# Kernel tuning notes

Measured on AMD Instinct MI355X. Metric: run time of the kernel, lower is better.

## Reference

```python
import jax, jax.numpy as jnp
import numpy as np

N, D = 16384, 512
C = 1024

def setup_inputs() -> dict:
    key = jax.random.key(0)
    k1, k2, k3 = jax.random.split(key, 3)
    inputs = jax.random.normal(k1, (N, D), dtype=jnp.float32)
    centers = jax.random.normal(k2, (C, D), dtype=jnp.float32)
    gamma = jnp.float32(1.0 / D)  # standard RBF bandwidth
    normalization = jax.random.normal(k3, (C, C), dtype=jnp.float32) * 0.02
    return {"inputs": inputs, "centers": centers, "gamma": gamma,
            "normalization": normalization}

def gaussian_kernel(inputs, centers, gamma):
    x2 = jnp.sum(inputs * inputs, axis=-1, keepdims=True)        # [N,1]
    c2 = jnp.sum(centers * centers, axis=-1)                     # [C]
    xc = jnp.einsum('nd,cd->nc', inputs, centers)                # [N,C]
    sq_dist = jnp.maximum(x2 + c2[None, :] - 2.0 * xc, 0.0)
    return jnp.exp(-gamma * sq_dist)                             # [N,C]

def reference(inputs, centers, gamma, normalization):
    inputs = inputs.reshape(inputs.shape[0], -1)
    densities = gaussian_kernel(inputs, centers, gamma)
    return densities @ normalization                             # [N,C]
```

## Files before the change

kernel.cpp:

```cpp
#include <hip/hip_runtime.h>
#include <hip/hip_bf16.h>
#include <stdint.h>

#define N_ROWS 16384
#define D_DIM  512
#define C_DIM  1024

typedef __attribute__((ext_vector_type(4))) float f32x4;
typedef __attribute__((ext_vector_type(8))) short bf16x8;

__device__ __forceinline__ short bfbits(float x) {
  uint32_t u = __float_as_uint(x);
  uint32_t r = (u + 0x7fffu + ((u >> 16) & 1u)) >> 16;
  return (short)r;
}

__device__ __forceinline__ void gload16(const short* g, const short* l) {
  __builtin_amdgcn_global_load_lds(
      (const __attribute__((address_space(1))) void*)g,
      (__attribute__((address_space(3))) void*)l, 16, 0, 0);
}

__global__ __launch_bounds__(256) void fused_prep(
    const float* __restrict__ inputs, const float* __restrict__ centers,
    const float* __restrict__ W, short* __restrict__ inb,
    short* __restrict__ cenb, short* __restrict__ wT,
    float* __restrict__ x2, float* __restrict__ c2) {
  int bid = blockIdx.x;
  if (bid < 4096 + 256) {
    const float* src; short* dst; float* sq; int row;
    if (bid < 4096) { src = inputs; dst = inb; sq = x2; row = bid * 4 + (threadIdx.x >> 6); }
    else { src = centers; dst = cenb; sq = c2; row = (bid - 4096) * 4 + (threadIdx.x >> 6); }
    int lane = threadIdx.x & 63;
    const float4* s = reinterpret_cast<const float4*>(src + (size_t)row * D_DIM) + lane * 2;
    float4 v0 = s[0], v1 = s[1];
    float ss = v0.x*v0.x + v0.y*v0.y + v0.z*v0.z + v0.w*v0.w
             + v1.x*v1.x + v1.y*v1.y + v1.z*v1.z + v1.w*v1.w;
    bf16x8 o;
    o[0]=bfbits(v0.x); o[1]=bfbits(v0.y); o[2]=bfbits(v0.z); o[3]=bfbits(v0.w);
    o[4]=bfbits(v1.x); o[5]=bfbits(v1.y); o[6]=bfbits(v1.z); o[7]=bfbits(v1.w);
    *reinterpret_cast<bf16x8*>(dst + (size_t)row * D_DIM + lane * 8) = o;
    #pragma unroll
    for (int off = 32; off; off >>= 1) ss += __shfl_down(ss, off, 64);
    if (lane == 0) sq[row] = ss;
  } else {
    __shared__ float tile[32][33];
    int b2 = bid - 4352;
    int j0 = (b2 & 31) * 32;
    int c0 = (b2 >> 5) * 32;
    int tx = threadIdx.x & 31;
    int ty = threadIdx.x >> 5;
    #pragma unroll
    for (int i = 0; i < 32; i += 8)
      tile[ty + i][tx] = W[(size_t)(c0 + ty + i) * C_DIM + j0 + tx];
    __syncthreads();
    #pragma unroll
    for (int i = 0; i < 32; i += 8)
      wT[(size_t)(j0 + ty + i) * C_DIM + c0 + tx] = bfbits(tile[tx][ty + i]);
  }
}

template<int EPI>
__global__ __launch_bounds__(512, 2)
void gemm256(const short* __restrict__ A, const short* __restrict__ B,
             void* __restrict__ Cp, const float* __restrict__ x2,
             const float* __restrict__ c2, const float* __restrict__ gptr,
             int K) {
  __shared__ __align__(16) short lds[65536];
  short* As = lds;
  short* Bs = lds + 32768;

  const int tid  = threadIdx.x;
  const int lane = tid & 63;
  const int wid  = tid >> 6;
  const int wr = wid >> 2;
  const int wc = wid & 3;

  const int bid  = blockIdx.x;
  const int brow = (bid & 7) * 8 + (bid >> 5);
  const int bcol = (bid >> 3) & 3;
  const int row0 = brow * 256, col0 = bcol * 256;

  const int NT = K >> 6;

  const int l15 = lane & 15;
  const int lk  = (lane >> 4) * 8;
  const int sw  = (lane & 7) << 3;
  const int swHi = sw & 32, swLo = sw & 24;
  const int ca0 = swHi | (lk ^ swLo);
  const int ca1 = (swHi ^ 32) | (lk ^ swLo);
  const int aRow = (wr * 128 + l15) * 64;
  const int bRow = (wc * 64  + l15) * 64;

  const int rowL = tid >> 3;
  const int chS  = ((tid & 7) ^ (rowL & 7)) << 3;
  const short* gA = A + (size_t)(row0 + rowL) * K + chS;
  const short* gB = B + (size_t)(col0 + rowL) * K + chS;
  const int ldsT = tid * 8;

#define STG_A(buf, u, kt) gload16(gA + (size_t)((u) * 64) * K + (kt), As + (buf) * 16384 + (u) * 4096 + ldsT)
#define STG_B(buf, u, kt) gload16(gB + (size_t)((u) * 64) * K + (kt), Bs + (buf) * 16384 + (u) * 4096 + ldsT)

  f32x4 acc[8][4] = {};

  STG_A(0, 0, 0); STG_A(0, 2, 0); STG_A(0, 1, 0); STG_A(0, 3, 0);
  STG_B(0, 0, 0); STG_B(0, 1, 0); STG_B(0, 2, 0); STG_B(0, 3, 0);
  {
    const int kt1 = ((NT > 1) ? 1 : 0) << 6;
    STG_A(1, 0, kt1); STG_A(1, 2, kt1);
    STG_B(1, 0, kt1); STG_B(1, 1, kt1); STG_B(1, 2, kt1); STG_B(1, 3, kt1);
  }
  asm volatile("s_waitcnt vmcnt(6)" ::: "memory");
  __builtin_amdgcn_s_barrier();

  bf16x8 a[4], b0[4], b1[4];
  for (int t = 0; t < NT; ++t) {
    const int bsel = t & 1, nb = bsel ^ 1;
    const short* aB = As + bsel * 16384;
    const short* bB = Bs + bsel * 16384;
    const int kt1 = ((t + 1 < NT) ? (t + 1) : (NT - 1)) << 6;
    const int kt2 = ((t + 2 < NT) ? (t + 2) : (NT - 1)) << 6;

    #pragma unroll
    for (int i = 0; i < 4; ++i) a[i]  = *(const bf16x8*)(aB + aRow + i * 1024 + ca0);
    #pragma unroll
    for (int n = 0; n < 4; ++n) b0[n] = *(const bf16x8*)(bB + bRow + n * 1024 + ca0);
    STG_A(nb, 1, kt1); STG_A(nb, 3, kt1);
    __builtin_amdgcn_s_barrier();
    asm volatile("s_waitcnt lgkmcnt(0)" ::: "memory");
    __builtin_amdgcn_sched_barrier(0);
    __builtin_amdgcn_s_setprio(1);
    #pragma unroll
    for (int i = 0; i < 4; ++i)
      #pragma unroll
      for (int n = 0; n < 4; ++n)
        acc[i][n] = __builtin_amdgcn_mfma_f32_16x16x32_bf16(a[i], b0[n], acc[i][n], 0, 0, 0);
    __builtin_amdgcn_s_setprio(0);
    __builtin_amdgcn_s_barrier();

    #pragma unroll
    for (int i = 0; i < 4; ++i) a[i] = *(const bf16x8*)(aB + aRow + (4 + i) * 1024 + ca0);
    __builtin_amdgcn_s_barrier();
    asm volatile("s_waitcnt lgkmcnt(0)" ::: "memory");
    __builtin_amdgcn_sched_barrier(0);
    __builtin_amdgcn_s_setprio(1);
    #pragma unroll
    for (int i = 0; i < 4; ++i)
      #pragma unroll
      for (int n = 0; n < 4; ++n)
        acc[4 + i][n] = __builtin_amdgcn_mfma_f32_16x16x32_bf16(a[i], b0[n], acc[4 + i][n], 0, 0, 0);
    __builtin_amdgcn_s_setprio(0);
    __builtin_amdgcn_s_barrier();

    #pragma unroll
    for (int i = 0; i < 4; ++i) a[i]  = *(const bf16x8*)(aB + aRow + i * 1024 + ca1);
    #pragma unroll
    for (int n = 0; n < 4; ++n) b1[n] = *(const bf16x8*)(bB + bRow + n * 1024 + ca1);
    __builtin_amdgcn_s_barrier();
    asm volatile("s_waitcnt lgkmcnt(0)" ::: "memory");
    __builtin_amdgcn_sched_barrier(0);
    __builtin_amdgcn_s_setprio(1);
    #pragma unroll
    for (int i = 0; i < 4; ++i)
      #pragma unroll
      for (int n = 0; n < 4; ++n)
        acc[i][n] = __builtin_amdgcn_mfma_f32_16x16x32_bf16(a[i], b1[n], acc[i][n], 0, 0, 0);
    __builtin_amdgcn_s_setprio(0);
    __builtin_amdgcn_s_barrier();

    #pragma unroll
    for (int i = 0; i < 4; ++i) a[i] = *(const bf16x8*)(aB + aRow + (4 + i) * 1024 + ca1);
    STG_A(bsel, 0, kt2); STG_A(bsel, 2, kt2);
    STG_B(bsel, 0, kt2); STG_B(bsel, 1, kt2); STG_B(bsel, 2, kt2); STG_B(bsel, 3, kt2);
    asm volatile("s_waitcnt vmcnt(6)" ::: "memory");
    __builtin_amdgcn_s_barrier();
    asm volatile("s_waitcnt lgkmcnt(0)" ::: "memory");
    __builtin_amdgcn_sched_barrier(0);
    __builtin_amdgcn_s_setprio(1);
    #pragma unroll
    for (int i = 0; i < 4; ++i)
      #pragma unroll
      for (int n = 0; n < 4; ++n)
        acc[4 + i][n] = __builtin_amdgcn_mfma_f32_16x16x32_bf16(a[i], b1[n], acc[4 + i][n], 0, 0, 0);
    __builtin_amdgcn_s_setprio(0);
    __builtin_amdgcn_s_barrier();
  }

  const int colB = col0 + wc * 64 + l15;
  const int rBase = row0 + wr * 128 + ((lane >> 4) << 2);

  if constexpr (EPI == 0) {
    short* Dm = (short*)Cp;
    const float g = *gptr;
    float cc2[4];
    #pragma unroll
    for (int n = 0; n < 4; ++n) cc2[n] = c2[colB + n * 16];
    #pragma unroll
    for (int m = 0; m < 8; ++m) {
      #pragma unroll
      for (int r = 0; r < 4; ++r) {
        const int row = rBase + m * 16 + r;
        const float xr = x2[row];
        size_t base = (size_t)row * C_DIM + colB;
        #pragma unroll
        for (int n = 0; n < 4; ++n) {
          float v = fmaxf(xr + cc2[n] - 2.0f * acc[m][n][r], 0.0f);
          Dm[base + n * 16] = bfbits(__expf(-g * v));
        }
      }
    }
  } else {
    float* Dm = (float*)Cp;
    #pragma unroll
    for (int m = 0; m < 8; ++m) {
      #pragma unroll
      for (int r = 0; r < 4; ++r) {
        const int row = rBase + m * 16 + r;
        size_t base = (size_t)row * C_DIM + colB;
        #pragma unroll
        for (int n = 0; n < 4; ++n)
          Dm[base + n * 16] = acc[m][n][r];
      }
    }
  }
#undef STG_A
#undef STG_B
}

extern "C" void kernel_launch(void* const* d_in, const int* in_sizes, int n_in,
                              void* d_out, int out_size, void* d_ws, size_t ws_size,
                              hipStream_t stream) {
  const float* inputs  = (const float*)d_in[0];
  const float* centers = (const float*)d_in[1];
  const float* gamma   = (const float*)d_in[2];
  const float* norm    = (const float*)d_in[3];
  float* out = (float*)d_out;

  char* ws = (char*)d_ws;
  short* inb  = (short*)(ws);
  short* cenb = (short*)(ws + (16u << 20));
  short* wT   = (short*)(ws + (17u << 20));
  float* x2   = (float*)(ws + (19u << 20));
  float* c2   = (float*)(ws + (19u << 20) + (1u << 16));
  short* dens = (short*)(ws + (20u << 20));

  fused_prep<<<5376, 256, 0, stream>>>(inputs, centers, norm, inb, cenb, wT, x2, c2);
  gemm256<0><<<256, 512, 0, stream>>>(inb, cenb, dens, x2, c2, gamma, D_DIM);
  gemm256<1><<<256, 512, 0, stream>>>(dens, wT, out, nullptr, nullptr, nullptr, C_DIM);
}
```

Measured before the change: 154.0 us.

## Replace ping-pong barrier schedule with simple double-buffered prefetch loop

Drops the finely interleaved GEMM main loop, which had partial-tile staggered global-to-LDS loads, per-phase barriers, lgkmcnt waits and s_setprio bumps. In its place is a plain double-buffer: the whole next tile is issued up front, all four MFMA phases run back to back, then the loop waits vmcnt(0) with one barrier per iteration. This removes most barrier and sync overhead and lets the compiler schedule the LDS reads freely. The cost is losing the two-tiles-ahead prefetch depth and the explicit wave-priority interleaving, so load latency may be hidden less well.

Measured after the change: 151.4 us. About the same (-1.7%).

```diff
diff --git a/kernel.cpp b/kernel.cpp
--- a/kernel.cpp
+++ b/kernel.cpp
@@ -100,90 +100,65 @@
 
 #define STG_A(buf, u, kt) gload16(gA + (size_t)((u) * 64) * K + (kt), As + (buf) * 16384 + (u) * 4096 + ldsT)
 #define STG_B(buf, u, kt) gload16(gB + (size_t)((u) * 64) * K + (kt), Bs + (buf) * 16384 + (u) * 4096 + ldsT)
+#define STG_TILE(buf, kt) do { \
+    STG_A(buf, 0, kt); STG_A(buf, 1, kt); STG_A(buf, 2, kt); STG_A(buf, 3, kt); \
+    STG_B(buf, 0, kt); STG_B(buf, 1, kt); STG_B(buf, 2, kt); STG_B(buf, 3, kt); \
+  } while (0)
 
   f32x4 acc[8][4] = {};
 
-  STG_A(0, 0, 0); STG_A(0, 2, 0); STG_A(0, 1, 0); STG_A(0, 3, 0);
-  STG_B(0, 0, 0); STG_B(0, 1, 0); STG_B(0, 2, 0); STG_B(0, 3, 0);
-  {
-    const int kt1 = ((NT > 1) ? 1 : 0) << 6;
-    STG_A(1, 0, kt1); STG_A(1, 2, kt1);
-    STG_B(1, 0, kt1); STG_B(1, 1, kt1); STG_B(1, 2, kt1); STG_B(1, 3, kt1);
-  }
-  asm volatile("s_waitcnt vmcnt(6)" ::: "memory");
+  STG_TILE(0, 0);
+  asm volatile("s_waitcnt vmcnt(0)" ::: "memory");
   __builtin_amdgcn_s_barrier();
-
-  bf16x8 a[4], b0[4], b1[4];
+  __builtin_amdgcn_sched_barrier(0);
+
   for (int t = 0; t < NT; ++t) {
     const int bsel = t & 1, nb = bsel ^ 1;
     const short* aB = As + bsel * 16384;
     const short* bB = Bs + bsel * 16384;
-    const int kt1 = ((t + 1 < NT) ? (t + 1) : (NT - 1)) << 6;
-    const int kt2 = ((t + 2 < NT) ? (t + 2) : (NT - 1)) << 6;
-
-    #pragma unroll
-    for (int i = 0; i < 4; ++i) a[i]  = *(const bf16x8*)(aB + aRow + i * 1024 + ca0);
+
+    if (t + 1 < NT) {
+      const int kt1 = (t + 1) << 6;
+      STG_TILE(nb, kt1);
+    }
+
+    bf16x8 a0[4], a1[4], b0[4], b1[4];
+    #pragma unroll
+    for (int i = 0; i < 4; ++i) a0[i] = *(const bf16x8*)(aB + aRow + i * 1024 + ca0);
     #pragma unroll
     for (int n = 0; n < 4; ++n) b0[n] = *(const bf16x8*)(bB + bRow + n * 1024 + ca0);
-    STG_A(nb, 1, kt1); STG_A(nb, 3, kt1);
+    #pragma unroll
+    for (int i = 0; i < 4; ++i)
+      #pragma unroll
+      for (int n = 0; n < 4; ++n)
+        acc[i][n] = __builtin_amdgcn_mfma_f32_16x16x32_bf16(a0[i], b0[n], acc[i][n], 0, 0, 0);
+    #pragma unroll
+    for (int i = 0; i < 4; ++i) a1[i] = *(const bf16x8*)(aB + aRow + (4 + i) * 1024 + ca0);
+    #pragma unroll
+    for (int i = 0; i < 4; ++i)
+      #pragma unroll
+      for (int n = 0; n < 4; ++n)
+        acc[4 + i][n] = __builtin_amdgcn_mfma_f32_16x16x32_bf16(a1[i], b0[n], acc[4 + i][n], 0, 0, 0);
+    #pragma unroll
+    for (int i = 0; i < 4; ++i) a0[i] = *(const bf16x8*)(aB + aRow + i * 1024 + ca1);
+    #pragma unroll
+    for (int n = 0; n < 4; ++n) b1[n] = *(const bf16x8*)(bB + bRow + n * 1024 + ca1);
+    #pragma unroll
+    for (int i = 0; i < 4; ++i)
+      #pragma unroll
+      for (int n = 0; n < 4; ++n)
+        acc[i][n] = __builtin_amdgcn_mfma_f32_16x16x32_bf16(a0[i], b1[n], acc[i][n], 0, 0, 0);
+    #pragma unroll
+    for (int i = 0; i < 4; ++i) a1[i] = *(const bf16x8*)(aB + aRow + (4 + i) * 1024 + ca1);
+    #pragma unroll
+    for (int i = 0; i < 4; ++i)
+      #pragma unroll
+      for (int n = 0; n < 4; ++n)
+        acc[4 + i][n] = __builtin_amdgcn_mfma_f32_16x16x32_bf16(a1[i], b1[n], acc[4 + i][n], 0, 0, 0);
+
+    asm volatile("s_waitcnt vmcnt(0)" ::: "memory");
     __builtin_amdgcn_s_barrier();
-    asm volatile("s_waitcnt lgkmcnt(0)" ::: "memory");
     __builtin_amdgcn_sched_barrier(0);
-    __builtin_amdgcn_s_setprio(1);
-    #pragma unroll
-    for (int i = 0; i < 4; ++i)
-      #pragma unroll
-      for (int n = 0; n < 4; ++n)
-        acc[i][n] = __builtin_amdgcn_mfma_f32_16x16x32_bf16(a[i], b0[n], acc[i][n], 0, 0, 0);
-    __builtin_amdgcn_s_setprio(0);
-    __builtin_amdgcn_s_barrier();
-
-    #pragma unroll
-    for (int i = 0; i < 4; ++i) a[i] = *(const bf16x8*)(aB + aRow + (4 + i) * 1024 + ca0);
-    __builtin_amdgcn_s_barrier();
-    asm volatile("s_waitcnt lgkmcnt(0)" ::: "memory");
-    __builtin_amdgcn_sched_barrier(0);
-    __builtin_amdgcn_s_setprio(1);
-    #pragma unroll
-    for (int i = 0; i < 4; ++i)
-      #pragma unroll
-      for (int n = 0; n < 4; ++n)
-        acc[4 + i][n] = __builtin_amdgcn_mfma_f32_16x16x32_bf16(a[i], b0[n], acc[4 + i][n], 0, 0, 0);
-    __builtin_amdgcn_s_setprio(0);
-    __builtin_amdgcn_s_barrier();
-
-    #pragma unroll
-    for (int i = 0; i < 4; ++i) a[i]  = *(const bf16x8*)(aB + aRow + i * 1024 + ca1);
-    #pragma unroll
-    for (int n = 0; n < 4; ++n) b1[n] = *(const bf16x8*)(bB + bRow + n * 1024 + ca1);
-    __builtin_amdgcn_s_barrier();
-    asm volatile("s_waitcnt lgkmcnt(0)" ::: "memory");
-    __builtin_amdgcn_sched_barrier(0);
-    __builtin_amdgcn_s_setprio(1);
-    #pragma unroll
-    for (int i = 0; i < 4; ++i)
-      #pragma unroll
-      for (int n = 0; n < 4; ++n)
-        acc[i][n] = __builtin_amdgcn_mfma_f32_16x16x32_bf16(a[i], b1[n], acc[i][n], 0, 0, 0);
-    __builtin_amdgcn_s_setprio(0);
-    __builtin_amdgcn_s_barrier();
-
-    #pragma unroll
-    for (int i = 0; i < 4; ++i) a[i] = *(const bf16x8*)(aB + aRow + (4 + i) * 1024 + ca1);
-    STG_A(bsel, 0, kt2); STG_A(bsel, 2, kt2);
-    STG_B(bsel, 0, kt2); STG_B(bsel, 1, kt2); STG_B(bsel, 2, kt2); STG_B(bsel, 3, kt2);
-    asm volatile("s_waitcnt vmcnt(6)" ::: "memory");
-    __builtin_amdgcn_s_barrier();
-    asm volatile("s_waitcnt lgkmcnt(0)" ::: "memory");
-    __builtin_amdgcn_sched_barrier(0);
-    __builtin_amdgcn_s_setprio(1);
-    #pragma unroll
-    for (int i = 0; i < 4; ++i)
-      #pragma unroll
-      for (int n = 0; n < 4; ++n)
-        acc[4 + i][n] = __builtin_amdgcn_mfma_f32_16x16x32_bf16(a[i], b1[n], acc[4 + i][n], 0, 0, 0);
-    __builtin_amdgcn_s_setprio(0);
-    __builtin_amdgcn_s_barrier();
   }
 
   const int colB = col0 + wc * 64 + l15;
@@ -225,6 +200,7 @@
   }
 #undef STG_A
 #undef STG_B
+#undef STG_TILE
 }
 
 extern "C" void kernel_launch(void* const* d_in, const int* in_sizes, int n_in,
```
